# Kernel tuning notes

Hardware: AMD Instinct MI355X
Metric: run time of the kernel (lower is better)

The kernel has to match this reference:

```python
import jax, jax.numpy as jnp
import numpy as np

B, T, D = 1, 1024, 2048
F_DIM = 1408
E = 8
TOPK = 2


def setup_inputs() -> dict:
    key = jax.random.key(0)
    ks = jax.random.split(key, 5)
    x = jax.random.normal(ks[0], (B, T, D), dtype=jnp.float32)
    # torch nn.Linear weight layout: [out_features, in_features]
    gate_w = jax.random.normal(ks[1], (E, D), dtype=jnp.float32) * 0.02
    gate_proj = jax.random.normal(ks[2], (E, F_DIM, D), dtype=jnp.float32) * 0.02
    up_proj = jax.random.normal(ks[3], (E, F_DIM, D), dtype=jnp.float32) * 0.02
    down_proj = jax.random.normal(ks[4], (E, D, F_DIM), dtype=jnp.float32) * 0.02
    return {"x": x, "gate_w": gate_w, "gate_proj": gate_proj,
            "up_proj": up_proj, "down_proj": down_proj}


def reference(x, gate_w, gate_proj, up_proj, down_proj):
    b, t, d = x.shape
    x_flat = x.reshape(-1, d)                                  # [N, D]
    n = x_flat.shape[0]
    # Router: top-k logits then softmax over the selected k.
    router_logits = x_flat @ gate_w.T                          # [N, E]
    top_w, sel = jax.lax.top_k(router_logits, TOPK)            # [N, K]
    top_w = jax.nn.softmax(top_w, axis=-1)                     # [N, K]
    # Scatter routing weights into dense per-token expert weights [N, E].
    tok_ids = jnp.arange(n)[:, None]
    tw = jnp.zeros((n, E), dtype=x.dtype).at[tok_ids, sel].add(top_w)
    # Dense expert compute (mathematically identical: unselected experts get
    # zero combine weight). SwiGLU per expert.
    g = jnp.einsum('nd,efd->enf', x_flat, gate_proj)           # [E, N, F]
    u = jnp.einsum('nd,efd->enf', x_flat, up_proj)             # [E, N, F]
    h = jax.nn.silu(g) * u                                     # [E, N, F]
    eo = jnp.einsum('enf,edf->end', h, down_proj)              # [E, N, D]
    out = jnp.einsum('end,ne->nd', eo, tw)                     # [N, D]
    return out.reshape(b, t, d)
```

## Files before the change

### kernel.cpp

```cpp
#include <hip/hip_runtime.h>
#include <hip/hip_bf16.h>
#include <stdint.h>

typedef __attribute__((ext_vector_type(8))) short short8;
typedef __attribute__((ext_vector_type(4))) float f32x4;
typedef unsigned int u32;
typedef unsigned short u16;

static constexpr int N_TOK = 1024;
static constexpr int DDIM = 2048;
static constexpr int FDIM = 1408;
static constexpr int NEXP = 8;
static constexpr int MAXROWS = 4096;
static constexpr int NT128 = 24;
static constexpr int NT256 = 16;

static constexpr size_t O_META   = 0;
static constexpr size_t O_TE128  = 256;
static constexpr size_t O_TR128  = 384;
static constexpr size_t O_TE256  = 512;
static constexpr size_t O_TR256  = 640;
static constexpr size_t O_ROWTOK = 768;
static constexpr size_t O_TOKROWS= O_ROWTOK + (size_t)MAXROWS * 4;
static constexpr size_t O_SEL    = O_TOKROWS + 2048 * 4;
static constexpr size_t O_W      = O_SEL + 2048 * 4;
static constexpr size_t O_XBF    = (O_W + 2048 * 4 + 255) & ~(size_t)255;
static constexpr size_t O_H      = O_XBF + (size_t)(N_TOK + 1) * DDIM * 2;
static constexpr size_t O_EO     = O_H + (size_t)MAXROWS * FDIM * 2;

static __device__ __forceinline__ u16 f2bf(float f) {
    return __builtin_bit_cast(u16, __float2bfloat16(f));
}
static __device__ __forceinline__ float bf2f(u16 s) {
    u32 u = ((u32)s) << 16;
    return __builtin_bit_cast(float, u);
}
static __device__ __forceinline__ u32 pack2(float a, float b) {
    return (u32)f2bf(a) | ((u32)f2bf(b) << 16);
}
static __device__ __forceinline__ void gload16(const void* g, void* l) {
    __builtin_amdgcn_global_load_lds(
        (const __attribute__((address_space(1))) void*)g,
        (__attribute__((address_space(3))) void*)l, 16, 0, 0);
}
#define PIN() __builtin_amdgcn_sched_barrier(0)
static __device__ __forceinline__ void sync_lgkm() {
    asm volatile("s_waitcnt lgkmcnt(0)" ::: "memory");
    __builtin_amdgcn_s_barrier();
    __builtin_amdgcn_sched_barrier(0);
}

__global__ __launch_bounds__(256) void router_kernel(
    const float* __restrict__ x, const float* __restrict__ gw,
    int* __restrict__ sel, float* __restrict__ wout, u16* __restrict__ xbf)
{
    __shared__ float xs[DDIM];
    __shared__ float lg[NEXP];
    const int tok = blockIdx.x;
    const float* xr = x + (size_t)tok * DDIM;
    for (int i = threadIdx.x; i < DDIM / 4; i += 256)
        ((float4*)xs)[i] = ((const float4*)xr)[i];
    __syncthreads();
    {
        const int i = threadIdx.x * 8;
        uint4 v;
        v.x = pack2(xs[i], xs[i + 1]);     v.y = pack2(xs[i + 2], xs[i + 3]);
        v.z = pack2(xs[i + 4], xs[i + 5]); v.w = pack2(xs[i + 6], xs[i + 7]);
        *(uint4*)(xbf + (size_t)tok * DDIM + i) = v;
        if (tok == 0)
            *(uint4*)(xbf + (size_t)N_TOK * DDIM + i) = uint4{0u, 0u, 0u, 0u};
    }
    const int wid = threadIdx.x >> 6, lane = threadIdx.x & 63;
    for (int i = 0; i < 2; i++) {
        const int e = wid * 2 + i;
        const float* g = gw + (size_t)e * DDIM;
        float s = 0.f;
        for (int k = lane; k < DDIM; k += 64) s += xs[k] * g[k];
        for (int off = 32; off > 0; off >>= 1) s += __shfl_down(s, off);
        if (lane == 0) lg[e] = s;
    }
    __syncthreads();
    if (threadIdx.x == 0) {
        int i1 = 0;
        for (int e = 1; e < NEXP; e++) if (lg[e] > lg[i1]) i1 = e;
        int i2 = -1;
        for (int e = 0; e < NEXP; e++) {
            if (e == i1) continue;
            if (i2 < 0 || lg[e] > lg[i2]) i2 = e;
        }
        const float e2 = __expf(lg[i2] - lg[i1]);
        const float w1 = 1.f / (1.f + e2);
        sel[tok * 2] = i1; sel[tok * 2 + 1] = i2;
        wout[tok * 2] = w1; wout[tok * 2 + 1] = e2 * w1;
    }
}

__global__ __launch_bounds__(512) void build_kernel(
    const int* __restrict__ sel,
    int* __restrict__ meta, int* __restrict__ te128, int* __restrict__ tr128,
    int* __restrict__ te256, int* __restrict__ tr256,
    int* __restrict__ row_tok, int* __restrict__ tok_rows)
{
    __shared__ int s0[N_TOK], s1[N_TOK];
    __shared__ u16 p0[N_TOK], p1[N_TOK];
    __shared__ int counts[NEXP], offs[NEXP];
    for (int i = threadIdx.x; i < N_TOK; i += 512) {
        s0[i] = sel[i * 2]; s1[i] = sel[i * 2 + 1];
    }
    __syncthreads();
    const int e = threadIdx.x >> 6, lane = threadIdx.x & 63;
    int base = 0;
    for (int c = 0; c < N_TOK / 64; c++) {
        const int tk = c * 64 + lane;
        const int slot = (s0[tk] == e) ? 0 : ((s1[tk] == e) ? 1 : -1);
        const unsigned long long m = __ballot(slot >= 0);
        const int pre = __popcll(m & ((1ull << lane) - 1ull));
        if (slot == 0) p0[tk] = (u16)(base + pre);
        else if (slot == 1) p1[tk] = (u16)(base + pre);
        base += __popcll(m);
    }
    if (lane == 0) counts[e] = base;
    __syncthreads();
    if (threadIdx.x == 0) {
        int off = 0, n128 = 0, n256 = 0;
        for (int qq = 0; qq < NEXP; qq++) {
            offs[qq] = off;
            const int cnt = counts[qq];
            const int pc = (cnt + 255) & ~255;
            for (int i = 0; i * 128 < cnt; i++) { te128[n128] = qq; tr128[n128] = off + i * 128; n128++; }
            for (int i = 0; i < pc / 256; i++)  { te256[n256] = qq; tr256[n256] = off + i * 256; n256++; }
            off += pc;
        }
        meta[0] = n128; meta[1] = off; meta[2] = n256;
    }
    __syncthreads();
    const int off = offs[e];
    for (int c = 0; c < N_TOK / 64; c++) {
        const int tk = c * 64 + lane;
        const int slot = (s0[tk] == e) ? 0 : ((s1[tk] == e) ? 1 : -1);
        if (slot >= 0) {
            const int row = off + (slot ? p1[tk] : p0[tk]);
            row_tok[row] = tk;
            tok_rows[tk * 2 + slot] = row;
        }
    }
    const int cnt = counts[e];
    const int pc = (cnt + 255) & ~255;
    for (int p = cnt + lane; p < pc; p += 64) row_tok[off + p] = -1;
}

__global__ __launch_bounds__(512, 4) void mlp1_kernel(
    const u16* __restrict__ xbf,
    const float* __restrict__ gp, const float* __restrict__ upw,
    u16* __restrict__ h,
    const int* __restrict__ meta, const int* __restrict__ te128,
    const int* __restrict__ tr128, const int* __restrict__ row_tok)
{
    const int tile = blockIdx.y;
    const int nb = blockIdx.x;
    if (tile >= meta[0]) return;
    const int n0 = nb * 32;
    const int e = te128[tile];
    const int r0g = tr128[tile];

    __shared__ __align__(16) u16 As[2][128 * 64];
    __shared__ __align__(16) u16 Bs0[2][32 * 64];
    __shared__ __align__(16) u16 Bs1[2][32 * 64];

    const int t = threadIdx.x;
    const int wid = t >> 6, lane = t & 63;
    const int lr = lane & 15, lhi = lane >> 4;
    const int wm = wid * 16;

    const u16* asrc[2];
    int aldsoff[2];
    #pragma unroll
    for (int j = 0; j < 2; j++) {
        const int row = wm + j * 8 + (lane >> 3);
        const int gran = (lane & 7) ^ (row & 7);
        const int tok = row_tok[r0g + row];
        asrc[j] = xbf + (size_t)(tok < 0 ? N_TOK : tok) * DDIM + gran * 8;
        aldsoff[j] = (wid * 2 + j) * 512;
    }

    const int rb = t >> 4, c4 = t & 15;
    const float* brow0 = gp  + (size_t)e * FDIM * DDIM + (size_t)(n0 + rb) * DDIM + c4 * 4;
    const float* brow1 = upw + (size_t)e * FDIM * DDIM + (size_t)(n0 + rb) * DDIM + c4 * 4;
    const int sOffB = rb * 64 + (((c4 >> 1) ^ (rb & 7)) * 8) + (c4 & 1) * 4;

    f32x4 acc0[2], acc1[2];
    acc0[0] = acc0[1] = acc1[0] = acc1[1] = f32x4{0.f, 0.f, 0.f, 0.f};
    float4 pb0P, pb1P, pb0Q, pb1Q;

    auto STAGEA = [&](int bsel, int k0) {
        #pragma unroll
        for (int j = 0; j < 2; j++)
            gload16(asrc[j] + k0, &As[bsel][aldsoff[j]]);
    };
    auto LOADB_P = [&](int k0) {
        pb0P = *(const float4*)(brow0 + k0);
        pb1P = *(const float4*)(brow1 + k0);
    };
    auto LOADB_Q = [&](int k0) {
        pb0Q = *(const float4*)(brow0 + k0);
        pb1Q = *(const float4*)(brow1 + k0);
    };
    auto STOREB_P = [&](int bsel) {
        uint2 v0; v0.x = pack2(pb0P.x, pb0P.y); v0.y = pack2(pb0P.z, pb0P.w);
        *(uint2*)(&Bs0[bsel][sOffB]) = v0;
        uint2 v1; v1.x = pack2(pb1P.x, pb1P.y); v1.y = pack2(pb1P.z, pb1P.w);
        *(uint2*)(&Bs1[bsel][sOffB]) = v1;
    };
    auto STOREB_Q = [&](int bsel) {
        uint2 v0; v0.x = pack2(pb0Q.x, pb0Q.y); v0.y = pack2(pb0Q.z, pb0Q.w);
        *(uint2*)(&Bs0[bsel][sOffB]) = v0;
        uint2 v1; v1.x = pack2(pb1Q.x, pb1Q.y); v1.y = pack2(pb1Q.z, pb1Q.w);
        *(uint2*)(&Bs1[bsel][sOffB]) = v1;
    };
    auto COMPUTE = [&](int bsel) {
        __builtin_amdgcn_s_setprio(1);
        #pragma unroll
        for (int ks = 0; ks < 2; ks++) {
            short8 a, b0[2], b1[2];
            {
                const int rowa = wm + lr;
                const int gr = (ks * 4 + lhi) ^ (rowa & 7);
                a = *(const short8*)(&As[bsel][rowa * 64 + gr * 8]);
            }
            #pragma unroll
            for (int n = 0; n < 2; n++) {
                const int rowb = n * 16 + lr;
                const int gr = (ks * 4 + lhi) ^ (rowb & 7);
                b0[n] = *(const short8*)(&Bs0[bsel][rowb * 64 + gr * 8]);
                b1[n] = *(const short8*)(&Bs1[bsel][rowb * 64 + gr * 8]);
            }
            #pragma unroll
            for (int n = 0; n < 2; n++) {
                acc0[n] = __builtin_amdgcn_mfma_f32_16x16x32_bf16(a, b0[n], acc0[n], 0, 0, 0);
                acc1[n] = __builtin_amdgcn_mfma_f32_16x16x32_bf16(a, b1[n], acc1[n], 0, 0, 0);
            }
        }
        __builtin_amdgcn_s_setprio(0);
    };

    constexpr int NT = DDIM / 64;
    STAGEA(0, 0);
    PIN();
    LOADB_P(0);
    LOADB_Q(64);
    PIN();
    STOREB_P(0);
    sync_lgkm();
    for (int kt = 0; kt < NT; kt += 2) {
        STAGEA(1, ((kt + 1) & (NT - 1)) * 64);
        PIN();
        LOADB_P(((kt + 2) & (NT - 1)) * 64);
        PIN();
        STOREB_Q(1);
        asm volatile("s_waitcnt vmcnt(4)" ::: "memory");
        PIN();
        COMPUTE(0);
        sync_lgkm();
        STAGEA(0, ((kt + 2) & (NT - 1)) * 64);
        PIN();
        LOADB_Q(((kt + 3) & (NT - 1)) * 64);
        PIN();
        STOREB_P(0);
        asm volatile("s_waitcnt vmcnt(4)" ::: "memory");
        PIN();
        COMPUTE(1);
        sync_lgkm();
    }

    #pragma unroll
    for (int n = 0; n < 2; n++) {
        const int col = n0 + n * 16 + lr;
        #pragma unroll
        for (int j = 0; j < 4; j++) {
            const int row = r0g + wm + lhi * 4 + j;
            const float g = acc0[n][j], u = acc1[n][j];
            const float hv = g / (1.f + __expf(-g)) * u;
            h[(size_t)row * FDIM + col] = f2bf(hv);
        }
    }
}

__global__ __launch_bounds__(1024, 8) void down_kernel(
    const u16* __restrict__ h, const float* __restrict__ dp,
    u16* __restrict__ eo,
    const int* __restrict__ meta, const int* __restrict__ te256,
    const int* __restrict__ tr256)
{
    const int tile = blockIdx.y;
    const int nb = blockIdx.x;
    if (tile >= meta[2]) return;
    const int n0 = nb * 64;
    const int e = te256[tile];
    const int r0g = tr256[tile];

    __shared__ __align__(16) u16 As[2][256 * 64];
    __shared__ __align__(16) u16 Bs[2][64 * 64];

    const int t = threadIdx.x;
    const int wid = t >> 6, lane = t & 63;
    const int lr = lane & 15, lhi = lane >> 4;
    const int wm = wid * 16;

    const u16* asrc[2];
    int aldsoff[2];
    #pragma unroll
    for (int j = 0; j < 2; j++) {
        const int row = wm + j * 8 + (lane >> 3);
        const int gran = (lane & 7) ^ (row & 7);
        asrc[j] = h + (size_t)(r0g + row) * FDIM + gran * 8;
        aldsoff[j] = (wid * 2 + j) * 512;
    }

    const int rb = t >> 4, c4 = t & 15;
    const float* brow = dp + (size_t)e * DDIM * FDIM + (size_t)(n0 + rb) * FDIM + c4 * 4;
    const int sOffB = rb * 64 + (((c4 >> 1) ^ (rb & 7)) * 8) + (c4 & 1) * 4;

    f32x4 acc[4];
    #pragma unroll
    for (int n = 0; n < 4; n++) acc[n] = f32x4{0.f,0.f,0.f,0.f};
    float4 pbP, pbQ;

    auto STAGEA = [&](int bsel, int k0) {
        #pragma unroll
        for (int j = 0; j < 2; j++)
            gload16(asrc[j] + k0, &As[bsel][aldsoff[j]]);
    };
    auto LOADB_P = [&](int k0) { pbP = *(const float4*)(brow + k0); };
    auto LOADB_Q = [&](int k0) { pbQ = *(const float4*)(brow + k0); };
    auto STOREB_P = [&](int bsel) {
        uint2 v; v.x = pack2(pbP.x, pbP.y); v.y = pack2(pbP.z, pbP.w);
        *(uint2*)(&Bs[bsel][sOffB]) = v;
    };
    auto STOREB_Q = [&](int bsel) {
        uint2 v; v.x = pack2(pbQ.x, pbQ.y); v.y = pack2(pbQ.z, pbQ.w);
        *(uint2*)(&Bs[bsel][sOffB]) = v;
    };
    auto COMPUTE = [&](int bsel) {
        __builtin_amdgcn_s_setprio(1);
        #pragma unroll
        for (int ks = 0; ks < 2; ks++) {
            short8 a;
            {
                const int rowa = wm + lr;
                const int gr = (ks * 4 + lhi) ^ (rowa & 7);
                a = *(const short8*)(&As[bsel][rowa * 64 + gr * 8]);
            }
            #pragma unroll
            for (int n = 0; n < 4; n++) {
                const int rowb = n * 16 + lr;
                const int gr = (ks * 4 + lhi) ^ (rowb & 7);
                const short8 b = *(const short8*)(&Bs[bsel][rowb * 64 + gr * 8]);
                acc[n] = __builtin_amdgcn_mfma_f32_16x16x32_bf16(a, b, acc[n], 0, 0, 0);
            }
        }
        __builtin_amdgcn_s_setprio(0);
    };

    constexpr int NT = FDIM / 64;
    STAGEA(0, 0);
    PIN();
    LOADB_P(0);
    LOADB_Q(64);
    PIN();
    STOREB_P(0);
    sync_lgkm();
    for (int kt = 0; kt < NT; kt += 2) {
        int k1 = kt + 1; if (k1 >= NT) k1 = 0;
        int k2 = kt + 2; if (k2 >= NT) k2 = 0;
        int k3 = kt + 3; if (k3 >= NT) k3 = 0;
        STAGEA(1, k1 * 64);
        PIN();
        LOADB_P(k2 * 64);
        PIN();
        STOREB_Q(1);
        asm volatile("s_waitcnt vmcnt(3)" ::: "memory");
        PIN();
        COMPUTE(0);
        sync_lgkm();
        STAGEA(0, k2 * 64);
        PIN();
        LOADB_Q(k3 * 64);
        PIN();
        STOREB_P(0);
        asm volatile("s_waitcnt vmcnt(3)" ::: "memory");
        PIN();
        COMPUTE(1);
        sync_lgkm();
    }

    #pragma unroll
    for (int n = 0; n < 4; n++) {
        const int col = n0 + n * 16 + lr;
        #pragma unroll
        for (int j = 0; j < 4; j++) {
            const int row = r0g + wm + lhi * 4 + j;
            eo[(size_t)row * DDIM + col] = f2bf(acc[n][j]);
        }
    }
}

__global__ __launch_bounds__(256) void combine_kernel(
    const u16* __restrict__ eo, const int* __restrict__ tok_rows,
    const float* __restrict__ w, float* __restrict__ out)
{
    const int tok = blockIdx.x;
    const int r1 = tok_rows[tok * 2], r2 = tok_rows[tok * 2 + 1];
    const float w1 = w[tok * 2], w2 = w[tok * 2 + 1];
    const int d = threadIdx.x * 8;
    const uint4 a = *(const uint4*)(eo + (size_t)r1 * DDIM + d);
    const uint4 b = *(const uint4*)(eo + (size_t)r2 * DDIM + d);
    const u32 av[4] = {a.x, a.y, a.z, a.w};
    const u32 bv[4] = {b.x, b.y, b.z, b.w};
    float4 o0, o1;
    float* op[8] = {&o0.x, &o0.y, &o0.z, &o0.w, &o1.x, &o1.y, &o1.z, &o1.w};
    #pragma unroll
    for (int i = 0; i < 4; i++) {
        *op[2 * i]     = w1 * bf2f((u16)(av[i] & 0xffff)) + w2 * bf2f((u16)(bv[i] & 0xffff));
        *op[2 * i + 1] = w1 * bf2f((u16)(av[i] >> 16))    + w2 * bf2f((u16)(bv[i] >> 16));
    }
    float4* po = (float4*)(out + (size_t)tok * DDIM + d);
    po[0] = o0; po[1] = o1;
}

extern "C" void kernel_launch(void* const* d_in, const int* in_sizes, int n_in,
                              void* d_out, int out_size, void* d_ws, size_t ws_size,
                              hipStream_t stream) {
    const float* x  = (const float*)d_in[0];
    const float* gw = (const float*)d_in[1];
    const float* gp = (const float*)d_in[2];
    const float* up = (const float*)d_in[3];
    const float* dp = (const float*)d_in[4];
    float* out = (float*)d_out;
    char* ws = (char*)d_ws;

    int*   meta     = (int*)(ws + O_META);
    int*   te128    = (int*)(ws + O_TE128);
    int*   tr128    = (int*)(ws + O_TR128);
    int*   te256    = (int*)(ws + O_TE256);
    int*   tr256    = (int*)(ws + O_TR256);
    int*   row_tok  = (int*)(ws + O_ROWTOK);
    int*   tok_rows = (int*)(ws + O_TOKROWS);
    int*   sel      = (int*)(ws + O_SEL);
    float* w        = (float*)(ws + O_W);
    u16*   xbf      = (u16*)(ws + O_XBF);
    u16*   h        = (u16*)(ws + O_H);
    u16*   eo       = (u16*)(ws + O_EO);

    router_kernel<<<N_TOK, 256, 0, stream>>>(x, gw, sel, w, xbf);
    build_kernel<<<1, 512, 0, stream>>>(sel, meta, te128, tr128, te256, tr256,
                                        row_tok, tok_rows);
    mlp1_kernel<<<dim3(FDIM / 32, NT128), 512, 0, stream>>>(
        xbf, gp, up, h, meta, te128, tr128, row_tok);
    down_kernel<<<dim3(DDIM / 64, NT256), 1024, 0, stream>>>(
        h, dp, eo, meta, te256, tr256);
    combine_kernel<<<N_TOK, 256, 0, stream>>>(eo, tok_rows, w, out);
}
```

Baseline: 183.1 us.

## Double mlp1 K-step to 128 per stage and pad 128-row tiles to 256

The gate/up GEMM kernel now processes a 128-wide K slice per pipeline stage (two 64-wide halves in LDS), halving the number of barrier/sync iterations and doubling loads in flight per stage. The wait counts rise to match, and launch bounds drop to 2 blocks per CU because LDS use doubles. Separately, the router now emits 128-row tiles covering the full 256-padded expert range (NT128 raised to 32), so the tile list follows the 256 padding. That may add work on padding rows.

```diff
diff --git a/kernel.cpp b/kernel.cpp
--- a/kernel.cpp
+++ b/kernel.cpp
@@ -12,7 +12,7 @@
 static constexpr int FDIM = 1408;
 static constexpr int NEXP = 8;
 static constexpr int MAXROWS = 4096;
-static constexpr int NT128 = 24;
+static constexpr int NT128 = 32;
 static constexpr int NT256 = 16;
 
 static constexpr size_t O_META   = 0;
@@ -125,10 +125,9 @@
         int off = 0, n128 = 0, n256 = 0;
         for (int qq = 0; qq < NEXP; qq++) {
             offs[qq] = off;
-            const int cnt = counts[qq];
-            const int pc = (cnt + 255) & ~255;
-            for (int i = 0; i * 128 < cnt; i++) { te128[n128] = qq; tr128[n128] = off + i * 128; n128++; }
-            for (int i = 0; i < pc / 256; i++)  { te256[n256] = qq; tr256[n256] = off + i * 256; n256++; }
+            const int pc = (counts[qq] + 255) & ~255;
+            for (int i = 0; i < pc / 128; i++) { te128[n128] = qq; tr128[n128] = off + i * 128; n128++; }
+            for (int i = 0; i < pc / 256; i++) { te256[n256] = qq; tr256[n256] = off + i * 256; n256++; }
             off += pc;
         }
         meta[0] = n128; meta[1] = off; meta[2] = n256;
@@ -149,7 +148,7 @@
     for (int p = cnt + lane; p < pc; p += 64) row_tok[off + p] = -1;
 }
 
-__global__ __launch_bounds__(512, 4) void mlp1_kernel(
+__global__ __launch_bounds__(512, 2) void mlp1_kernel(
     const u16* __restrict__ xbf,
     const float* __restrict__ gp, const float* __restrict__ upw,
     u16* __restrict__ h,
@@ -163,9 +162,9 @@
     const int e = te128[tile];
     const int r0g = tr128[tile];
 
-    __shared__ __align__(16) u16 As[2][128 * 64];
-    __shared__ __align__(16) u16 Bs0[2][32 * 64];
-    __shared__ __align__(16) u16 Bs1[2][32 * 64];
+    __shared__ __align__(16) u16 As[2][2][128 * 64];
+    __shared__ __align__(16) u16 Bs0[2][2][32 * 64];
+    __shared__ __align__(16) u16 Bs1[2][2][32 * 64];
 
     const int t = threadIdx.x;
     const int wid = t >> 6, lane = t & 63;
@@ -190,83 +189,99 @@
 
     f32x4 acc0[2], acc1[2];
     acc0[0] = acc0[1] = acc1[0] = acc1[1] = f32x4{0.f, 0.f, 0.f, 0.f};
-    float4 pb0P, pb1P, pb0Q, pb1Q;
+    float4 p0aP, p0bP, p1aP, p1bP;
+    float4 p0aQ, p0bQ, p1aQ, p1bQ;
 
     auto STAGEA = [&](int bsel, int k0) {
         #pragma unroll
-        for (int j = 0; j < 2; j++)
-            gload16(asrc[j] + k0, &As[bsel][aldsoff[j]]);
+        for (int j = 0; j < 2; j++) {
+            gload16(asrc[j] + k0,      &As[bsel][0][aldsoff[j]]);
+            gload16(asrc[j] + k0 + 64, &As[bsel][1][aldsoff[j]]);
+        }
     };
     auto LOADB_P = [&](int k0) {
-        pb0P = *(const float4*)(brow0 + k0);
-        pb1P = *(const float4*)(brow1 + k0);
+        p0aP = *(const float4*)(brow0 + k0);      p0bP = *(const float4*)(brow0 + k0 + 64);
+        p1aP = *(const float4*)(brow1 + k0);      p1bP = *(const float4*)(brow1 + k0 + 64);
     };
     auto LOADB_Q = [&](int k0) {
-        pb0Q = *(const float4*)(brow0 + k0);
-        pb1Q = *(const float4*)(brow1 + k0);
+        p0aQ = *(const float4*)(brow0 + k0);      p0bQ = *(const float4*)(brow0 + k0 + 64);
+        p1aQ = *(const float4*)(brow1 + k0);      p1bQ = *(const float4*)(brow1 + k0 + 64);
     };
     auto STOREB_P = [&](int bsel) {
-        uint2 v0; v0.x = pack2(pb0P.x, pb0P.y); v0.y = pack2(pb0P.z, pb0P.w);
-        *(uint2*)(&Bs0[bsel][sOffB]) = v0;
-        uint2 v1; v1.x = pack2(pb1P.x, pb1P.y); v1.y = pack2(pb1P.z, pb1P.w);
-        *(uint2*)(&Bs1[bsel][sOffB]) = v1;
+        uint2 v;
+        v.x = pack2(p0aP.x, p0aP.y); v.y = pack2(p0aP.z, p0aP.w);
+        *(uint2*)(&Bs0[bsel][0][sOffB]) = v;
+        v.x = pack2(p0bP.x, p0bP.y); v.y = pack2(p0bP.z, p0bP.w);
+        *(uint2*)(&Bs0[bsel][1][sOffB]) = v;
+        v.x = pack2(p1aP.x, p1aP.y); v.y = pack2(p1aP.z, p1aP.w);
+        *(uint2*)(&Bs1[bsel][0][sOffB]) = v;
+        v.x = pack2(p1bP.x, p1bP.y); v.y = pack2(p1bP.z, p1bP.w);
+        *(uint2*)(&Bs1[bsel][1][sOffB]) = v;
     };
     auto STOREB_Q = [&](int bsel) {
-        uint2 v0; v0.x = pack2(pb0Q.x, pb0Q.y); v0.y = pack2(pb0Q.z, pb0Q.w);
-        *(uint2*)(&Bs0[bsel][sOffB]) = v0;
-        uint2 v1; v1.x = pack2(pb1Q.x, pb1Q.y); v1.y = pack2(pb1Q.z, pb1Q.w);
-        *(uint2*)(&Bs1[bsel][sOffB]) = v1;
+        uint2 v;
+        v.x = pack2(p0aQ.x, p0aQ.y); v.y = pack2(p0aQ.z, p0aQ.w);
+        *(uint2*)(&Bs0[bsel][0][sOffB]) = v;
+        v.x = pack2(p0bQ.x, p0bQ.y); v.y = pack2(p0bQ.z, p0bQ.w);
+        *(uint2*)(&Bs0[bsel][1][sOffB]) = v;
+        v.x = pack2(p1aQ.x, p1aQ.y); v.y = pack2(p1aQ.z, p1aQ.w);
+        *(uint2*)(&Bs1[bsel][0][sOffB]) = v;
+        v.x = pack2(p1bQ.x, p1bQ.y); v.y = pack2(p1bQ.z, p1bQ.w);
+        *(uint2*)(&Bs1[bsel][1][sOffB]) = v;
     };
     auto COMPUTE = [&](int bsel) {
         __builtin_amdgcn_s_setprio(1);
         #pragma unroll
-        for (int ks = 0; ks < 2; ks++) {
-            short8 a, b0[2], b1[2];
-            {
-                const int rowa = wm + lr;
-                const int gr = (ks * 4 + lhi) ^ (rowa & 7);
-                a = *(const short8*)(&As[bsel][rowa * 64 + gr * 8]);
+        for (int half = 0; half < 2; half++) {
+            #pragma unroll
+            for (int ksl = 0; ksl < 2; ksl++) {
+                short8 a, b0[2], b1[2];
+                {
+                    const int rowa = wm + lr;
+                    const int gr = (ksl * 4 + lhi) ^ (rowa & 7);
+                    a = *(const short8*)(&As[bsel][half][rowa * 64 + gr * 8]);
+                }
+                #pragma unroll
+                for (int n = 0; n < 2; n++) {
+                    const int rowb = n * 16 + lr;
+                    const int gr = (ksl * 4 + lhi) ^ (rowb & 7);
+                    b0[n] = *(const short8*)(&Bs0[bsel][half][rowb * 64 + gr * 8]);
+                    b1[n] = *(const short8*)(&Bs1[bsel][half][rowb * 64 + gr * 8]);
+                }
+                #pragma unroll
+                for (int n = 0; n < 2; n++) {
+                    acc0[n] = __builtin_amdgcn_mfma_f32_16x16x32_bf16(a, b0[n], acc0[n], 0, 0, 0);
+                    acc1[n] = __builtin_amdgcn_mfma_f32_16x16x32_bf16(a, b1[n], acc1[n], 0, 0, 0);
+                }
             }
-            #pragma unroll
-            for (int n = 0; n < 2; n++) {
-                const int rowb = n * 16 + lr;
-                const int gr = (ks * 4 + lhi) ^ (rowb & 7);
-                b0[n] = *(const short8*)(&Bs0[bsel][rowb * 64 + gr * 8]);
-                b1[n] = *(const short8*)(&Bs1[bsel][rowb * 64 + gr * 8]);
-            }
-            #pragma unroll
-            for (int n = 0; n < 2; n++) {
-                acc0[n] = __builtin_amdgcn_mfma_f32_16x16x32_bf16(a, b0[n], acc0[n], 0, 0, 0);
-                acc1[n] = __builtin_amdgcn_mfma_f32_16x16x32_bf16(a, b1[n], acc1[n], 0, 0, 0);
-            }
         }
         __builtin_amdgcn_s_setprio(0);
     };
 
-    constexpr int NT = DDIM / 64;
+    constexpr int NT = DDIM / 128;
     STAGEA(0, 0);
     PIN();
     LOADB_P(0);
-    LOADB_Q(64);
+    LOADB_Q(128);
     PIN();
     STOREB_P(0);
     sync_lgkm();
     for (int kt = 0; kt < NT; kt += 2) {
-        STAGEA(1, ((kt + 1) & (NT - 1)) * 64);
-        PIN();
-        LOADB_P(((kt + 2) & (NT - 1)) * 64);
+        STAGEA(1, ((kt + 1) & (NT - 1)) * 128);
+        PIN();
+        LOADB_P(((kt + 2) & (NT - 1)) * 128);
         PIN();
         STOREB_Q(1);
-        asm volatile("s_waitcnt vmcnt(4)" ::: "memory");
+        asm volatile("s_waitcnt vmcnt(8)" ::: "memory");
         PIN();
         COMPUTE(0);
         sync_lgkm();
-        STAGEA(0, ((kt + 2) & (NT - 1)) * 64);
-        PIN();
-        LOADB_Q(((kt + 3) & (NT - 1)) * 64);
+        STAGEA(0, ((kt + 2) & (NT - 1)) * 128);
+        PIN();
+        LOADB_Q(((kt + 3) & (NT - 1)) * 128);
         PIN();
         STOREB_P(0);
-        asm volatile("s_waitcnt vmcnt(4)" ::: "memory");
+        asm volatile("s_waitcnt vmcnt(8)" ::: "memory");
         PIN();
         COMPUTE(1);
         sync_lgkm();
```

After: 223.8 us. +22.2%, slower.
